# Kernel tuning notes

Hardware: AMD Instinct MI355X
Metric: run time of the kernel (lower is better)

The kernel has to match this reference:

```python
import jax, jax.numpy as jnp
import numpy as np

B, H, S, D = 4, 12, 2048, 64


def setup_inputs() -> dict:
    key = jax.random.key(0)
    k1, k2, k3 = jax.random.split(key, 3)
    keys = jax.random.normal(k1, (B, H, S, D), dtype=jnp.float32)
    queries = jax.random.normal(k2, (B, H, S, D), dtype=jnp.float32)
    values = jax.random.normal(k3, (B, H, S, D), dtype=jnp.float32)
    return {"keys": keys, "queries": queries, "values": values}


def reference(keys, queries, values):
    d_k = keys.shape[-1]
    # scores: [B, H, S, S]
    scores = jnp.einsum("bhqd,bhkd->bhqk", queries, keys) / jnp.sqrt(jnp.asarray(d_k, dtype=scores_dtype(queries)))
    s = scores.shape[-1]
    causal = jnp.triu(jnp.ones((s, s), dtype=bool), k=1)  # True above diagonal -> masked
    scores = jnp.where(causal, -jnp.inf, scores)
    attn = jax.nn.softmax(scores, axis=-1)
    return jnp.einsum("bhqk,bhkd->bhqd", attn, values)


def scores_dtype(x):
    return x.dtype
```

## Files before the change

### kernel.cpp

```cpp
#include <hip/hip_runtime.h>
#include <hip/hip_bf16.h>

#define B_SZ 4
#define H_SZ 12
#define S_LEN 2048
#define DH 64
#define KT 64
#define NQT (S_LEN / 64)
#define NQT2 (NQT / 2)
#define M2 9.0f

typedef _Float16 half8 __attribute__((ext_vector_type(8)));
typedef _Float16 half4v __attribute__((ext_vector_type(4)));
typedef float f32x4 __attribute__((ext_vector_type(4)));

__device__ __forceinline__ int gk_swz(int row) { return ((row & 3) << 1) | ((row >> 3) & 1); }
__device__ __forceinline__ int gv_swz(int d) { return (d & 7) ^ ((d >> 3) & 7); }

#define GLOAD_LDS16(gp, lp)                                                              \
    __builtin_amdgcn_global_load_lds(                                                    \
        (const __attribute__((address_space(1))) void*)(gp),                             \
        (__attribute__((address_space(3))) void*)(lp), 16, 0, 0)

__global__ __launch_bounds__(256) void cvt_pre(
    const float* __restrict__ Kg, const float* __restrict__ Vg,
    _Float16* __restrict__ wsK, _Float16* __restrict__ wsV)
{
    const int blk = blockIdx.x;
    const size_t gbase = (size_t)blk * (64 * 64);
    const int t = threadIdx.x;

    __shared__ float vt[64 * 65];

#pragma unroll
    for (int i = 0; i < 4; ++i) {
        int f = t + 256 * i;
        int row = f >> 4, c4 = (f & 15) << 2;
        float4 v = *(const float4*)(Vg + gbase + row * 64 + c4);
        vt[row * 65 + c4 + 0] = v.x; vt[row * 65 + c4 + 1] = v.y;
        vt[row * 65 + c4 + 2] = v.z; vt[row * 65 + c4 + 3] = v.w;
    }

#pragma unroll
    for (int i = 0; i < 2; ++i) {
        int u = t + 256 * i;
        int row = u >> 3, p = u & 7;
        int s = p ^ gk_swz(row);
        float4 x = *(const float4*)(Kg + gbase + row * 64 + s * 8);
        float4 y = *(const float4*)(Kg + gbase + row * 64 + s * 8 + 4);
        half8 h;
        h[0]=(_Float16)x.x; h[1]=(_Float16)x.y; h[2]=(_Float16)x.z; h[3]=(_Float16)x.w;
        h[4]=(_Float16)y.x; h[5]=(_Float16)y.y; h[6]=(_Float16)y.z; h[7]=(_Float16)y.w;
        *(half8*)&wsK[(size_t)blk * 4096 + row * 64 + p * 8] = h;
    }

    __syncthreads();

#pragma unroll
    for (int i = 0; i < 2; ++i) {
        int u = t + 256 * i;
        int d = u >> 3, p = u & 7;
        int s = p ^ gv_swz(d);
        half8 h;
#pragma unroll
        for (int e = 0; e < 8; ++e) h[e] = (_Float16)vt[(s * 8 + e) * 65 + d];
        *(half8*)&wsV[(size_t)blk * 4096 + d * 64 + p * 8] = h;
    }
}

__global__ __launch_bounds__(256, 3) void fa_fwd_ws(
    const _Float16* __restrict__ wsK,
    const _Float16* __restrict__ wsV,
    const float* __restrict__ Qg,
    float* __restrict__ Og)
{
    const int bh = blockIdx.x;
    const int y  = blockIdx.y;
    const int qt = (y & 1) ? (y >> 1) : (NQT2 - 1 - (y >> 1));
    const size_t base = (size_t)bh * S_LEN * DH;

    const int tid  = threadIdx.x;
    const int wave = tid >> 6;
    const int lane = tid & 63;
    const int l16  = lane & 15;
    const int quad = lane >> 4;

    __shared__ __align__(16) _Float16 Klds[2][128 * 64];
    __shared__ __align__(16) _Float16 Vlds[2 * 64 * 64];

    const int rlo = qt * 128 + wave * 32;

    const float qs = 0.125f * 1.44269504f;
    half8 qlo[2], qhi[2];
    {
        const float* plo = Qg + base + (size_t)(rlo + l16) * DH + quad * 8;
        const float* phi = plo + 16 * DH;
#pragma unroll
        for (int c = 0; c < 2; ++c) {
            float4 x = *(const float4*)(plo + c * 32);
            float4 y4 = *(const float4*)(plo + c * 32 + 4);
            half8 f;
            f[0]=(_Float16)(x.x*qs); f[1]=(_Float16)(x.y*qs); f[2]=(_Float16)(x.z*qs); f[3]=(_Float16)(x.w*qs);
            f[4]=(_Float16)(y4.x*qs); f[5]=(_Float16)(y4.y*qs); f[6]=(_Float16)(y4.z*qs); f[7]=(_Float16)(y4.w*qs);
            qlo[c] = f;
            x = *(const float4*)(phi + c * 32);
            y4 = *(const float4*)(phi + c * 32 + 4);
            f[0]=(_Float16)(x.x*qs); f[1]=(_Float16)(x.y*qs); f[2]=(_Float16)(x.z*qs); f[3]=(_Float16)(x.w*qs);
            f[4]=(_Float16)(y4.x*qs); f[5]=(_Float16)(y4.y*qs); f[6]=(_Float16)(y4.z*qs); f[7]=(_Float16)(y4.w*qs);
            qhi[c] = f;
        }
    }

    auto stageK = [&](int bb, int rnd) {
        const size_t toff = ((size_t)(bh * 32 + 2 * rnd)) << 13;
        const char* s = (const char*)wsK + toff + wave * 1024 + lane * 16;
        char* d = (char*)&Klds[bb][0] + wave * 1024;
#pragma unroll
        for (int i = 0; i < 4; ++i) GLOAD_LDS16(s + i * 4096, d + i * 4096);
    };
    auto stageV = [&](int rnd) {
        const size_t toff = ((size_t)(bh * 32 + 2 * rnd)) << 13;
        const char* s = (const char*)wsV + toff + wave * 1024 + lane * 16;
        char* d = (char*)&Vlds[0] + wave * 1024;
#pragma unroll
        for (int i = 0; i < 4; ++i) GLOAD_LDS16(s + i * 4096, d + i * 4096);
    };

    f32x4 olo[4], ohi[4];
#pragma unroll
    for (int t = 0; t < 4; ++t) { olo[t] = f32x4{0.f,0.f,0.f,0.f}; ohi[t] = f32x4{0.f,0.f,0.f,0.f}; }
    f32x4 llo = f32x4{0.f,0.f,0.f,0.f}, lhi = f32x4{0.f,0.f,0.f,0.f};
    const half8 ones = {(_Float16)1.f,(_Float16)1.f,(_Float16)1.f,(_Float16)1.f,
                        (_Float16)1.f,(_Float16)1.f,(_Float16)1.f,(_Float16)1.f};

    const int kr0 = ((l16 >> 2) << 3) + (l16 & 3);
    const int klq = quad * 8;
    const int qrl = (wave << 5) + l16;
    const int qrh = qrl + 16;

    auto kfrag = [&](int b, int cd, int t) -> half8 {
        int row = kr0 + ((t & 1) << 2) + ((t >> 1) << 5);
        int p = (((cd << 2) + quad) ^ gk_swz(row));
        return *(const half8*)&Klds[b][row * 64 + (p << 3)];
    };
    auto vfrag = [&](int c, int t) -> half8 {
        int d = l16 + 16 * t;
        int p = ((((c & 1) << 2) + quad) ^ gv_swz(d));
        return *(const half8*)&Vlds[(c >> 1) * 4096 + d * 64 + (p << 3)];
    };

    const int niter = qt + 1;
    int b = 0;
    stageK(0, 0);
    for (int it = 0; it < niter; ++it) {
        __syncthreads();
        if (it + 1 < niter) stageK(b ^ 1, it + 1);
        stageV(it);
        asm volatile("" ::: "memory");

        f32x4 sl[8], sh[8];
#pragma unroll
        for (int t = 0; t < 8; ++t) { sl[t] = f32x4{0.f,0.f,0.f,0.f}; sh[t] = f32x4{0.f,0.f,0.f,0.f}; }
        __builtin_amdgcn_s_setprio(1);
#pragma unroll
        for (int cd = 0; cd < 2; ++cd)
#pragma unroll
            for (int t = 0; t < 8; ++t) {
                half8 kf = kfrag(b, cd, t);
                sl[t] = __builtin_amdgcn_mfma_f32_16x16x32_f16(kf, qlo[cd], sl[t], 0, 0, 0);
                sh[t] = __builtin_amdgcn_mfma_f32_16x16x32_f16(kf, qhi[cd], sh[t], 0, 0, 0);
            }
        __builtin_amdgcn_s_setprio(0);
        if (it == niter - 1) {
#pragma unroll
            for (int t = 0; t < 8; ++t)
#pragma unroll
                for (int r = 0; r < 4; ++r) {
                    int k = klq + ((t & 1) << 2) + ((t >> 1) << 5) + r;
                    if (k > qrl) sl[t][r] = -1e30f;
                    if (k > qrh) sh[t][r] = -1e30f;
                }
        }
#pragma unroll
        for (int t = 0; t < 8; ++t)
#pragma unroll
            for (int r = 0; r < 4; ++r) {
                sl[t][r] = __builtin_amdgcn_exp2f(sl[t][r] - M2);
                sh[t][r] = __builtin_amdgcn_exp2f(sh[t][r] - M2);
            }
        half8 pal[4], pah[4];
#pragma unroll
        for (int c = 0; c < 4; ++c) {
            half8 pa;
            f32x4 s0 = sl[2 * c], s1 = sl[2 * c + 1];
            pa[0]=(_Float16)s0[0]; pa[1]=(_Float16)s0[1]; pa[2]=(_Float16)s0[2]; pa[3]=(_Float16)s0[3];
            pa[4]=(_Float16)s1[0]; pa[5]=(_Float16)s1[1]; pa[6]=(_Float16)s1[2]; pa[7]=(_Float16)s1[3];
            pal[c] = pa;
            s0 = sh[2 * c]; s1 = sh[2 * c + 1];
            pa[0]=(_Float16)s0[0]; pa[1]=(_Float16)s0[1]; pa[2]=(_Float16)s0[2]; pa[3]=(_Float16)s0[3];
            pa[4]=(_Float16)s1[0]; pa[5]=(_Float16)s1[1]; pa[6]=(_Float16)s1[2]; pa[7]=(_Float16)s1[3];
            pah[c] = pa;
        }

        __syncthreads();

        __builtin_amdgcn_s_setprio(1);
#pragma unroll
        for (int c = 0; c < 4; ++c) {
            llo = __builtin_amdgcn_mfma_f32_16x16x32_f16(ones, pal[c], llo, 0, 0, 0);
            lhi = __builtin_amdgcn_mfma_f32_16x16x32_f16(ones, pah[c], lhi, 0, 0, 0);
#pragma unroll
            for (int t = 0; t < 4; ++t) {
                half8 vb = vfrag(c, t);
                olo[t] = __builtin_amdgcn_mfma_f32_16x16x32_f16(vb, pal[c], olo[t], 0, 0, 0);
                ohi[t] = __builtin_amdgcn_mfma_f32_16x16x32_f16(vb, pah[c], ohi[t], 0, 0, 0);
            }
        }
        __builtin_amdgcn_s_setprio(0);
        b ^= 1;
    }

    const float il = 1.0f / llo[0];
    const float ih = 1.0f / lhi[0];
#pragma unroll
    for (int t = 0; t < 4; ++t) {
        *(f32x4*)(Og + base + (size_t)(rlo + l16) * DH + 16 * t + quad * 4) = olo[t] * il;
        *(f32x4*)(Og + base + (size_t)(rlo + 16 + l16) * DH + 16 * t + quad * 4) = ohi[t] * ih;
    }
}

__global__ __launch_bounds__(256, 3) void fa_fwd_legacy(
    const float* __restrict__ Kg,
    const float* __restrict__ Qg,
    const float* __restrict__ Vg,
    float* __restrict__ Og)
{
    const int bh = blockIdx.x;
    const int j  = blockIdx.y;
    const size_t base = (size_t)bh * S_LEN * DH;

    const int tid  = threadIdx.x;
    const int wave = tid >> 6;
    const int lane = tid & 63;
    const int l16  = lane & 15;
    const int quad = lane >> 4;

    __shared__ __align__(16) _Float16 Klds[2][KT * 72];
    __shared__ __align__(16) _Float16 Vlds[2][DH * 64];

    const int rlo = j * 64 + wave * 16;
    const int rhi = (NQT - 1 - j) * 64 + wave * 16;

    const float qs = 0.125f * 1.44269504f;
    half8 qlo[2], qhi[2];
    {
        const float* plo = Qg + base + (size_t)(rlo + l16) * DH + quad * 8;
        const float* phi = Qg + base + (size_t)(rhi + l16) * DH + quad * 8;
#pragma unroll
        for (int c = 0; c < 2; ++c) {
            float4 x = *(const float4*)(plo + c * 32);
            float4 y = *(const float4*)(plo + c * 32 + 4);
            half8 f;
            f[0]=(_Float16)(x.x*qs); f[1]=(_Float16)(x.y*qs); f[2]=(_Float16)(x.z*qs); f[3]=(_Float16)(x.w*qs);
            f[4]=(_Float16)(y.x*qs); f[5]=(_Float16)(y.y*qs); f[6]=(_Float16)(y.z*qs); f[7]=(_Float16)(y.w*qs);
            qlo[c] = f;
            x = *(const float4*)(phi + c * 32);
            y = *(const float4*)(phi + c * 32 + 4);
            f[0]=(_Float16)(x.x*qs); f[1]=(_Float16)(x.y*qs); f[2]=(_Float16)(x.z*qs); f[3]=(_Float16)(x.w*qs);
            f[4]=(_Float16)(y.x*qs); f[5]=(_Float16)(y.y*qs); f[6]=(_Float16)(y.z*qs); f[7]=(_Float16)(y.w*qs);
            qhi[c] = f;
        }
    }

    float4 kreg[4];
    float  vreg[16];

    auto load_tile = [&](int kv0) {
#pragma unroll
        for (int i = 0; i < 4; ++i) {
            int f = tid + 256 * i;
            kreg[i] = *(const float4*)(Kg + base + (size_t)(kv0 + (f >> 4)) * DH + ((f & 15) << 2));
        }
        const float* vp = Vg + base + (size_t)(kv0 + wave * 16) * DH + lane;
#pragma unroll
        for (int jj = 0; jj < 16; ++jj) vreg[jj] = vp[jj * DH];
    };
    auto cvt_store = [&](int b) {
#pragma unroll
        for (int i = 0; i < 4; ++i) {
            int f = tid + 256 * i;
            half4v hk = {(_Float16)kreg[i].x, (_Float16)kreg[i].y,
                         (_Float16)kreg[i].z, (_Float16)kreg[i].w};
            *(half4v*)&Klds[b][(f >> 4) * 72 + ((f & 15) << 2)] = hk;
        }
        half8 lo, hi;
#pragma unroll
        for (int jj = 0; jj < 8; ++jj) { lo[jj] = (_Float16)vreg[jj]; hi[jj] = (_Float16)vreg[jj + 8]; }
        _Float16* vrow = &Vlds[b][lane * 64];
        *(half8*)&vrow[(((2 * wave + 0) ^ (lane & 7)) << 3)] = lo;
        *(half8*)&vrow[(((2 * wave + 1) ^ (lane & 7)) << 3)] = hi;
    };

    f32x4 olo[4], ohi[4];
#pragma unroll
    for (int t = 0; t < 4; ++t) { olo[t] = f32x4{0.f,0.f,0.f,0.f}; ohi[t] = f32x4{0.f,0.f,0.f,0.f}; }
    f32x4 llo = f32x4{0.f,0.f,0.f,0.f}, lhi = f32x4{0.f,0.f,0.f,0.f};
    const half8 ones = {(_Float16)1.f,(_Float16)1.f,(_Float16)1.f,(_Float16)1.f,
                        (_Float16)1.f,(_Float16)1.f,(_Float16)1.f,(_Float16)1.f};

    const int kr0    = ((l16 >> 2) << 3) + (l16 & 3);
    const int qrow64 = wave * 16 + l16;
    const int klq    = quad * 8;

    auto kfrag = [&](int b, int c, int t) -> half8 {
        return *(const half8*)&Klds[b][(kr0 + ((t & 1) << 2) + ((t >> 1) << 5)) * 72 + c * 32 + quad * 8];
    };
    auto vfrag = [&](int b, int c, int t) -> half8 {
        int d = l16 + 16 * t;
        return *(const half8*)&Vlds[b][d * 64 + ((((c << 2) + quad) ^ (d & 7)) << 3)];
    };
    auto mask_diag = [&](f32x4* sc) {
#pragma unroll
        for (int t = 0; t < 4; ++t)
#pragma unroll
            for (int r = 0; r < 4; ++r)
                if (klq + ((t & 1) << 2) + ((t >> 1) << 5) + r > qrow64) sc[t][r] = -1e30f;
    };
    auto exp_all = [&](f32x4* sc) {
#pragma unroll
        for (int t = 0; t < 4; ++t)
#pragma unroll
            for (int r = 0; r < 4; ++r)
                sc[t][r] = __builtin_amdgcn_exp2f(sc[t][r] - M2);
    };
    auto pack_pa = [&](const f32x4* sc, int c) -> half8 {
        half8 pa;
        const f32x4 s0 = sc[2 * c], s1 = sc[2 * c + 1];
        pa[0] = (_Float16)s0[0]; pa[1] = (_Float16)s0[1];
        pa[2] = (_Float16)s0[2]; pa[3] = (_Float16)s0[3];
        pa[4] = (_Float16)s1[0]; pa[5] = (_Float16)s1[1];
        pa[6] = (_Float16)s1[2]; pa[7] = (_Float16)s1[3];
        return pa;
    };

    auto do_single = [&](int b, const half8* qf, f32x4* oacc, f32x4& lacc, bool diag) {
        f32x4 sc[4];
#pragma unroll
        for (int t = 0; t < 4; ++t) sc[t] = f32x4{0.f,0.f,0.f,0.f};
#pragma unroll
        for (int c = 0; c < 2; ++c)
#pragma unroll
            for (int t = 0; t < 4; ++t)
                sc[t] = __builtin_amdgcn_mfma_f32_16x16x32_f16(kfrag(b, c, t), qf[c], sc[t], 0, 0, 0);
        if (diag) mask_diag(sc);
        exp_all(sc);
#pragma unroll
        for (int c = 0; c < 2; ++c) {
            half8 pa = pack_pa(sc, c);
            lacc = __builtin_amdgcn_mfma_f32_16x16x32_f16(ones, pa, lacc, 0, 0, 0);
#pragma unroll
            for (int t = 0; t < 4; ++t)
                oacc[t] = __builtin_amdgcn_mfma_f32_16x16x32_f16(vfrag(b, c, t), pa, oacc[t], 0, 0, 0);
        }
    };

    auto do_dual = [&](int b, bool dlo) {
        f32x4 sh[4], sl[4];
#pragma unroll
        for (int t = 0; t < 4; ++t) { sh[t] = f32x4{0.f,0.f,0.f,0.f}; sl[t] = f32x4{0.f,0.f,0.f,0.f}; }
#pragma unroll
        for (int c = 0; c < 2; ++c)
#pragma unroll
            for (int t = 0; t < 4; ++t) {
                half8 kf = kfrag(b, c, t);
                sh[t] = __builtin_amdgcn_mfma_f32_16x16x32_f16(kf, qhi[c], sh[t], 0, 0, 0);
                sl[t] = __builtin_amdgcn_mfma_f32_16x16x32_f16(kf, qlo[c], sl[t], 0, 0, 0);
            }
        if (dlo) mask_diag(sl);
        exp_all(sh);
        exp_all(sl);
#pragma unroll
        for (int c = 0; c < 2; ++c) {
            half8 ph = pack_pa(sh, c);
            half8 pl = pack_pa(sl, c);
            lhi = __builtin_amdgcn_mfma_f32_16x16x32_f16(ones, ph, lhi, 0, 0, 0);
            llo = __builtin_amdgcn_mfma_f32_16x16x32_f16(ones, pl, llo, 0, 0, 0);
#pragma unroll
            for (int t = 0; t < 4; ++t) {
                half8 vb = vfrag(b, c, t);
                ohi[t] = __builtin_amdgcn_mfma_f32_16x16x32_f16(vb, ph, ohi[t], 0, 0, 0);
                olo[t] = __builtin_amdgcn_mfma_f32_16x16x32_f16(vb, pl, olo[t], 0, 0, 0);
            }
        }
    };

    const int niter = NQT - j;
    load_tile(0);
    int b = 0;
    for (int it = 0; it < niter; ++it) {
        cvt_store(b);
        __syncthreads();
        if (it + 1 < niter) load_tile((it + 1) * KT);
        asm volatile("" ::: "memory");
        if (it <= j) do_dual(b, it == j);
        else         do_single(b, qhi, ohi, lhi, it == niter - 1);
        b ^= 1;
    }

    const float il = 1.0f / llo[0];
    const float ih = 1.0f / lhi[0];
#pragma unroll
    for (int t = 0; t < 4; ++t) {
        *(f32x4*)(Og + base + (size_t)(rlo + l16) * DH + 16 * t + quad * 4) = olo[t] * il;
        *(f32x4*)(Og + base + (size_t)(rhi + l16) * DH + 16 * t + quad * 4) = ohi[t] * ih;
    }
}

extern "C" void kernel_launch(void* const* d_in, const int* in_sizes, int n_in,
                              void* d_out, int out_size, void* d_ws, size_t ws_size,
                              hipStream_t stream) {
    const float* K = (const float*)d_in[0];
    const float* Q = (const float*)d_in[1];
    const float* V = (const float*)d_in[2];
    float* O = (float*)d_out;

    const size_t halfs_per_tensor = (size_t)B_SZ * H_SZ * S_LEN * DH;
    const size_t ws_needed = 2 * halfs_per_tensor * sizeof(_Float16);

    if (d_ws != nullptr && ws_size >= ws_needed) {
        _Float16* wsK = (_Float16*)d_ws;
        _Float16* wsV = wsK + halfs_per_tensor;
        cvt_pre<<<dim3(B_SZ * H_SZ * NQT), dim3(256), 0, stream>>>(K, V, wsK, wsV);
        dim3 grid(B_SZ * H_SZ, NQT2);
        fa_fwd_ws<<<grid, dim3(256), 0, stream>>>(wsK, wsV, Q, O);
    } else {
        dim3 grid(B_SZ * H_SZ, NQT / 2);
        fa_fwd_legacy<<<grid, dim3(256), 0, stream>>>(K, Q, V, O);
    }
}
```

Measured before the change: 161.1 us.

## Replace LDS-staged attention kernel with single-wave blocks loading K/V fragments directly

The attention kernel now runs one wave per block, with each block owning 32 query rows. K and V fragments are loaded straight from global memory (L2/L1) into registers instead of being staged through double-buffered LDS with global_load_lds and barriers. The conversion kernel drops the XOR swizzles, since LDS bank conflicts no longer matter. This removes LDS traffic and __syncthreads, but gives up reuse of K/V tiles across the waves of a block and depends on cache hit rates for repeated global fragment loads.

```diff
diff --git a/kernel.cpp b/kernel.cpp
--- a/kernel.cpp
+++ b/kernel.cpp
@@ -7,20 +7,11 @@
 #define DH 64
 #define KT 64
 #define NQT (S_LEN / 64)
-#define NQT2 (NQT / 2)
 #define M2 9.0f
 
 typedef _Float16 half8 __attribute__((ext_vector_type(8)));
 typedef _Float16 half4v __attribute__((ext_vector_type(4)));
 typedef float f32x4 __attribute__((ext_vector_type(4)));
-
-__device__ __forceinline__ int gk_swz(int row) { return ((row & 3) << 1) | ((row >> 3) & 1); }
-__device__ __forceinline__ int gv_swz(int d) { return (d & 7) ^ ((d >> 3) & 7); }
-
-#define GLOAD_LDS16(gp, lp)                                                              \
-    __builtin_amdgcn_global_load_lds(                                                    \
-        (const __attribute__((address_space(1))) void*)(gp),                             \
-        (__attribute__((address_space(3))) void*)(lp), 16, 0, 0)
 
 __global__ __launch_bounds__(256) void cvt_pre(
     const float* __restrict__ Kg, const float* __restrict__ Vg,
@@ -45,9 +36,8 @@
     for (int i = 0; i < 2; ++i) {
         int u = t + 256 * i;
         int row = u >> 3, p = u & 7;
-        int s = p ^ gk_swz(row);
-        float4 x = *(const float4*)(Kg + gbase + row * 64 + s * 8);
-        float4 y = *(const float4*)(Kg + gbase + row * 64 + s * 8 + 4);
+        float4 x = *(const float4*)(Kg + gbase + row * 64 + p * 8);
+        float4 y = *(const float4*)(Kg + gbase + row * 64 + p * 8 + 4);
         half8 h;
         h[0]=(_Float16)x.x; h[1]=(_Float16)x.y; h[2]=(_Float16)x.z; h[3]=(_Float16)x.w;
         h[4]=(_Float16)y.x; h[5]=(_Float16)y.y; h[6]=(_Float16)y.z; h[7]=(_Float16)y.w;
@@ -60,15 +50,14 @@
     for (int i = 0; i < 2; ++i) {
         int u = t + 256 * i;
         int d = u >> 3, p = u & 7;
-        int s = p ^ gv_swz(d);
         half8 h;
 #pragma unroll
-        for (int e = 0; e < 8; ++e) h[e] = (_Float16)vt[(s * 8 + e) * 65 + d];
+        for (int e = 0; e < 8; ++e) h[e] = (_Float16)vt[(p * 8 + e) * 65 + d];
         *(half8*)&wsV[(size_t)blk * 4096 + d * 64 + p * 8] = h;
     }
 }
 
-__global__ __launch_bounds__(256, 3) void fa_fwd_ws(
+__global__ __launch_bounds__(64, 4) void fa_fwd_reg(
     const _Float16* __restrict__ wsK,
     const _Float16* __restrict__ wsV,
     const float* __restrict__ Qg,
@@ -76,24 +65,18 @@
 {
     const int bh = blockIdx.x;
     const int y  = blockIdx.y;
-    const int qt = (y & 1) ? (y >> 1) : (NQT2 - 1 - (y >> 1));
+    const int qw = (y & 1) ? (y >> 1) : (63 - (y >> 1));
     const size_t base = (size_t)bh * S_LEN * DH;
 
-    const int tid  = threadIdx.x;
-    const int wave = tid >> 6;
-    const int lane = tid & 63;
+    const int lane = threadIdx.x & 63;
     const int l16  = lane & 15;
     const int quad = lane >> 4;
-
-    __shared__ __align__(16) _Float16 Klds[2][128 * 64];
-    __shared__ __align__(16) _Float16 Vlds[2 * 64 * 64];
-
-    const int rlo = qt * 128 + wave * 32;
+    const int r0   = qw * 32;
 
     const float qs = 0.125f * 1.44269504f;
     half8 qlo[2], qhi[2];
     {
-        const float* plo = Qg + base + (size_t)(rlo + l16) * DH + quad * 8;
+        const float* plo = Qg + base + (size_t)(r0 + l16) * DH + quad * 8;
         const float* phi = plo + 16 * DH;
 #pragma unroll
         for (int c = 0; c < 2; ++c) {
@@ -111,21 +94,6 @@
         }
     }
 
-    auto stageK = [&](int bb, int rnd) {
-        const size_t toff = ((size_t)(bh * 32 + 2 * rnd)) << 13;
-        const char* s = (const char*)wsK + toff + wave * 1024 + lane * 16;
-        char* d = (char*)&Klds[bb][0] + wave * 1024;
-#pragma unroll
-        for (int i = 0; i < 4; ++i) GLOAD_LDS16(s + i * 4096, d + i * 4096);
-    };
-    auto stageV = [&](int rnd) {
-        const size_t toff = ((size_t)(bh * 32 + 2 * rnd)) << 13;
-        const char* s = (const char*)wsV + toff + wave * 1024 + lane * 16;
-        char* d = (char*)&Vlds[0] + wave * 1024;
-#pragma unroll
-        for (int i = 0; i < 4; ++i) GLOAD_LDS16(s + i * 4096, d + i * 4096);
-    };
-
     f32x4 olo[4], ohi[4];
 #pragma unroll
     for (int t = 0; t < 4; ++t) { olo[t] = f32x4{0.f,0.f,0.f,0.f}; ohi[t] = f32x4{0.f,0.f,0.f,0.f}; }
@@ -135,97 +103,80 @@
 
     const int kr0 = ((l16 >> 2) << 3) + (l16 & 3);
     const int klq = quad * 8;
-    const int qrl = (wave << 5) + l16;
-    const int qrh = qrl + 16;
-
-    auto kfrag = [&](int b, int cd, int t) -> half8 {
-        int row = kr0 + ((t & 1) << 2) + ((t >> 1) << 5);
-        int p = (((cd << 2) + quad) ^ gk_swz(row));
-        return *(const half8*)&Klds[b][row * 64 + (p << 3)];
-    };
-    auto vfrag = [&](int c, int t) -> half8 {
-        int d = l16 + 16 * t;
-        int p = ((((c & 1) << 2) + quad) ^ gv_swz(d));
-        return *(const half8*)&Vlds[(c >> 1) * 4096 + d * 64 + (p << 3)];
-    };
-
-    const int niter = qt + 1;
-    int b = 0;
-    stageK(0, 0);
-    for (int it = 0; it < niter; ++it) {
-        __syncthreads();
-        if (it + 1 < niter) stageK(b ^ 1, it + 1);
-        stageV(it);
-        asm volatile("" ::: "memory");
-
-        f32x4 sl[8], sh[8];
-#pragma unroll
-        for (int t = 0; t < 8; ++t) { sl[t] = f32x4{0.f,0.f,0.f,0.f}; sh[t] = f32x4{0.f,0.f,0.f,0.f}; }
-        __builtin_amdgcn_s_setprio(1);
-#pragma unroll
-        for (int cd = 0; cd < 2; ++cd)
-#pragma unroll
-            for (int t = 0; t < 8; ++t) {
-                half8 kf = kfrag(b, cd, t);
-                sl[t] = __builtin_amdgcn_mfma_f32_16x16x32_f16(kf, qlo[cd], sl[t], 0, 0, 0);
-                sh[t] = __builtin_amdgcn_mfma_f32_16x16x32_f16(kf, qhi[cd], sh[t], 0, 0, 0);
+    const int qrd = ((qw & 1) << 5) + l16;
+
+    const _Float16* kb0 = wsK + ((size_t)bh * 32) * 4096;
+    const _Float16* vb0 = wsV + ((size_t)bh * 32) * 4096;
+
+    const int ntile = (qw >> 1) + 1;
+    for (int kt = 0; kt < ntile; ++kt) {
+        const _Float16* kb = kb0 + kt * 4096;
+        const _Float16* vb = vb0 + kt * 4096;
+        const bool diag = (kt == ntile - 1);
+#pragma unroll
+        for (int ct = 0; ct < 2; ++ct) {
+            if (diag && (qw & 1) == 0 && ct == 1) continue;
+
+            half8 kf[4];
+#pragma unroll
+            for (int cd = 0; cd < 2; ++cd)
+#pragma unroll
+                for (int tt = 0; tt < 2; ++tt)
+                    kf[cd * 2 + tt] =
+                        *(const half8*)&kb[(kr0 + (tt << 2) + (ct << 5)) * 64 + cd * 32 + quad * 8];
+
+            f32x4 sl[2], sh[2];
+            sl[0] = f32x4{0.f,0.f,0.f,0.f}; sl[1] = f32x4{0.f,0.f,0.f,0.f};
+            sh[0] = f32x4{0.f,0.f,0.f,0.f}; sh[1] = f32x4{0.f,0.f,0.f,0.f};
+#pragma unroll
+            for (int cd = 0; cd < 2; ++cd)
+#pragma unroll
+                for (int tt = 0; tt < 2; ++tt) {
+                    sl[tt] = __builtin_amdgcn_mfma_f32_16x16x32_f16(kf[cd*2+tt], qlo[cd], sl[tt], 0, 0, 0);
+                    sh[tt] = __builtin_amdgcn_mfma_f32_16x16x32_f16(kf[cd*2+tt], qhi[cd], sh[tt], 0, 0, 0);
+                }
+
+            if (diag && ct == (qw & 1)) {
+#pragma unroll
+                for (int tt = 0; tt < 2; ++tt)
+#pragma unroll
+                    for (int r = 0; r < 4; ++r) {
+                        int k = klq + (tt << 2) + r + (ct << 5);
+                        if (k > qrd)      sl[tt][r] = -1e30f;
+                        if (k > qrd + 16) sh[tt][r] = -1e30f;
+                    }
             }
-        __builtin_amdgcn_s_setprio(0);
-        if (it == niter - 1) {
-#pragma unroll
-            for (int t = 0; t < 8; ++t)
+
+#pragma unroll
+            for (int tt = 0; tt < 2; ++tt)
 #pragma unroll
                 for (int r = 0; r < 4; ++r) {
-                    int k = klq + ((t & 1) << 2) + ((t >> 1) << 5) + r;
-                    if (k > qrl) sl[t][r] = -1e30f;
-                    if (k > qrh) sh[t][r] = -1e30f;
+                    sl[tt][r] = __builtin_amdgcn_exp2f(sl[tt][r] - M2);
+                    sh[tt][r] = __builtin_amdgcn_exp2f(sh[tt][r] - M2);
                 }
-        }
-#pragma unroll
-        for (int t = 0; t < 8; ++t)
-#pragma unroll
-            for (int r = 0; r < 4; ++r) {
-                sl[t][r] = __builtin_amdgcn_exp2f(sl[t][r] - M2);
-                sh[t][r] = __builtin_amdgcn_exp2f(sh[t][r] - M2);
+            half8 pl, ph;
+            pl[0]=(_Float16)sl[0][0]; pl[1]=(_Float16)sl[0][1]; pl[2]=(_Float16)sl[0][2]; pl[3]=(_Float16)sl[0][3];
+            pl[4]=(_Float16)sl[1][0]; pl[5]=(_Float16)sl[1][1]; pl[6]=(_Float16)sl[1][2]; pl[7]=(_Float16)sl[1][3];
+            ph[0]=(_Float16)sh[0][0]; ph[1]=(_Float16)sh[0][1]; ph[2]=(_Float16)sh[0][2]; ph[3]=(_Float16)sh[0][3];
+            ph[4]=(_Float16)sh[1][0]; ph[5]=(_Float16)sh[1][1]; ph[6]=(_Float16)sh[1][2]; ph[7]=(_Float16)sh[1][3];
+
+            llo = __builtin_amdgcn_mfma_f32_16x16x32_f16(ones, pl, llo, 0, 0, 0);
+            lhi = __builtin_amdgcn_mfma_f32_16x16x32_f16(ones, ph, lhi, 0, 0, 0);
+#pragma unroll
+            for (int t4 = 0; t4 < 4; ++t4) {
+                half8 vf = *(const half8*)&vb[(l16 + 16 * t4) * 64 + (ct << 5) + quad * 8];
+                olo[t4] = __builtin_amdgcn_mfma_f32_16x16x32_f16(vf, pl, olo[t4], 0, 0, 0);
+                ohi[t4] = __builtin_amdgcn_mfma_f32_16x16x32_f16(vf, ph, ohi[t4], 0, 0, 0);
             }
-        half8 pal[4], pah[4];
-#pragma unroll
-        for (int c = 0; c < 4; ++c) {
-            half8 pa;
-            f32x4 s0 = sl[2 * c], s1 = sl[2 * c + 1];
-            pa[0]=(_Float16)s0[0]; pa[1]=(_Float16)s0[1]; pa[2]=(_Float16)s0[2]; pa[3]=(_Float16)s0[3];
-            pa[4]=(_Float16)s1[0]; pa[5]=(_Float16)s1[1]; pa[6]=(_Float16)s1[2]; pa[7]=(_Float16)s1[3];
-            pal[c] = pa;
-            s0 = sh[2 * c]; s1 = sh[2 * c + 1];
-            pa[0]=(_Float16)s0[0]; pa[1]=(_Float16)s0[1]; pa[2]=(_Float16)s0[2]; pa[3]=(_Float16)s0[3];
-            pa[4]=(_Float16)s1[0]; pa[5]=(_Float16)s1[1]; pa[6]=(_Float16)s1[2]; pa[7]=(_Float16)s1[3];
-            pah[c] = pa;
-        }
-
-        __syncthreads();
-
-        __builtin_amdgcn_s_setprio(1);
-#pragma unroll
-        for (int c = 0; c < 4; ++c) {
-            llo = __builtin_amdgcn_mfma_f32_16x16x32_f16(ones, pal[c], llo, 0, 0, 0);
-            lhi = __builtin_amdgcn_mfma_f32_16x16x32_f16(ones, pah[c], lhi, 0, 0, 0);
-#pragma unroll
-            for (int t = 0; t < 4; ++t) {
-                half8 vb = vfrag(c, t);
-                olo[t] = __builtin_amdgcn_mfma_f32_16x16x32_f16(vb, pal[c], olo[t], 0, 0, 0);
-                ohi[t] = __builtin_amdgcn_mfma_f32_16x16x32_f16(vb, pah[c], ohi[t], 0, 0, 0);
-            }
-        }
-        __builtin_amdgcn_s_setprio(0);
-        b ^= 1;
+        }
     }
 
     const float il = 1.0f / llo[0];
     const float ih = 1.0f / lhi[0];
 #pragma unroll
     for (int t = 0; t < 4; ++t) {
-        *(f32x4*)(Og + base + (size_t)(rlo + l16) * DH + 16 * t + quad * 4) = olo[t] * il;
-        *(f32x4*)(Og + base + (size_t)(rlo + 16 + l16) * DH + 16 * t + quad * 4) = ohi[t] * ih;
+        *(f32x4*)(Og + base + (size_t)(r0 + l16) * DH + 16 * t + quad * 4) = olo[t] * il;
+        *(f32x4*)(Og + base + (size_t)(r0 + 16 + l16) * DH + 16 * t + quad * 4) = ohi[t] * ih;
     }
 }
 
@@ -431,8 +382,8 @@
         _Float16* wsK = (_Float16*)d_ws;
         _Float16* wsV = wsK + halfs_per_tensor;
         cvt_pre<<<dim3(B_SZ * H_SZ * NQT), dim3(256), 0, stream>>>(K, V, wsK, wsV);
-        dim3 grid(B_SZ * H_SZ, NQT2);
-        fa_fwd_ws<<<grid, dim3(256), 0, stream>>>(wsK, wsV, Q, O);
+        dim3 grid(B_SZ * H_SZ, 64);
+        fa_fwd_reg<<<grid, dim3(64), 0, stream>>>(wsK, wsV, Q, O);
     } else {
         dim3 grid(B_SZ * H_SZ, NQT / 2);
         fa_fwd_legacy<<<grid, dim3(256), 0, stream>>>(K, Q, V, O);
```

Measured after the change: 215.9 us. 1.34x slower.
